# Optimization experiments

Hardware: AMD Instinct MI355X
Metric: run time of the kernel (lower is better)

## Reference

```python
import jax, jax.numpy as jnp
import numpy as np
import math

B, N, T_DIM, K, G = 4, 96, 512, 12, 8


def _normalize(x, eps=1e-6):
    n = jnp.linalg.norm(x, axis=-1, keepdims=True)
    return x / jnp.maximum(n, eps)


def setup_inputs():
    key = jax.random.key(0)
    ks = jax.random.split(key, 12)
    chest_raw = jnp.array([[-0.707, 0.0, 0.707], [0.0, 0.0, 1.0], [0.438, 0.0, 0.899],
                           [0.707, 0.0, 0.707], [0.899, 0.0, 0.438], [0.966, 0.0, 0.259]],
                          dtype=jnp.float32)
    return {
        "mu": jax.random.uniform(ks[0], (B, N), dtype=jnp.float32),
        "sigma0": jax.random.normal(ks[1], (B, N), dtype=jnp.float32) * 0.5,
        "sigma_vel": jax.random.normal(ks[2], (B, N), dtype=jnp.float32) * 0.1,
        "amplitude": jax.random.normal(ks[3], (B, N), dtype=jnp.float32),
        "sh_base": jax.random.normal(ks[4], (B, N, 9), dtype=jnp.float32) * 0.5,
        "sh_vel": jax.random.normal(ks[5], (B, N, 9), dtype=jnp.float32) * 0.1,
        "p0": jax.random.normal(ks[6], (B, N, 3), dtype=jnp.float32) * 0.5,
        "p_vel": jax.random.normal(ks[7], (B, N, 3), dtype=jnp.float32) * 0.2,
        "splat_tau_raw": jnp.asarray(0.0, dtype=jnp.float32),
        "dist_atten_raw": jnp.asarray(-0.5, dtype=jnp.float32),
        "limb_ra": jnp.zeros(3, dtype=jnp.float32),
        "limb_la": jnp.array([1.0, 0.0, 0.0], dtype=jnp.float32),
        "limb_ll": jnp.array([0.5, math.sqrt(3.0) / 2.0, 0.0], dtype=jnp.float32),
        "chest_vectors": chest_raw / jnp.linalg.norm(chest_raw, axis=-1, keepdims=True),
        "conv1_w": jax.random.normal(ks[8], (32, 2, 3, 3), dtype=jnp.float32) * 0.2,
        "conv1_b": jnp.zeros(32, dtype=jnp.float32),
        "conv2_w": jax.random.normal(ks[9], (32, 32, 3, 3), dtype=jnp.float32) * 0.06,
        "conv2_b": jnp.zeros(32, dtype=jnp.float32),
        "fc_w": jax.random.normal(ks[10], (1, 32), dtype=jnp.float32) * 0.2,
        "fc_b": jnp.zeros(1, dtype=jnp.float32),
        "T": T_DIM,
    }


def _conv3x3(x, w, b):
    y = jax.lax.conv_general_dilated(x, w, (1, 1), 'SAME',
                                     dimension_numbers=('NCHW', 'OIHW', 'NCHW'))
    return y + b[None, :, None, None]


def reference(mu, sigma0, sigma_vel, amplitude, sh_base, sh_vel, p0, p_vel,
              splat_tau_raw, dist_atten_raw, limb_ra, limb_la, limb_ll, chest_vectors,
              conv1_w, conv1_b, conv2_w, conv2_b, fc_w, fc_b, T):
    Bq, Nq = mu.shape
    # temporal Gaussian profile
    t = jnp.linspace(0.0, 1.0, T)                                   # (T,)
    dt = t[None, None, :] - mu[:, :, None]                          # (B,N,T)
    sigma_t = jax.nn.softplus(sigma0[:, :, None] + sigma_vel[:, :, None] * dt) + 1e-3
    gauss = amplitude[:, :, None] * jnp.exp(-0.5 * (dt / sigma_t) ** 2)   # (B,N,T)
    sh_dyn = sh_base[:, :, None, :] + sh_vel[:, :, None, :] * dt[..., None]  # (B,N,T,9)

    # dipole position inside the open unit ball
    p_raw = p0[:, :, None, :] + p_vel[:, :, None, :] * dt[..., None]      # (B,N,T,3)
    nrm = jnp.maximum(jnp.linalg.norm(p_raw, axis=-1, keepdims=True), 1e-8)
    p_pos = p_raw / nrm * jnp.tanh(nrm)                                   # (B,N,T,3)

    # limb lead axes from Einthoven triangle (derived every forward)
    L_I = _normalize(limb_la - limb_ra)
    L_II = _normalize(limb_ll - limb_ra)
    L_III = _normalize(limb_ll - limb_la)
    L_aVR = _normalize(limb_ra - (limb_la + limb_ll) * 0.5)
    L_aVL = _normalize(limb_la - (limb_ra + limb_ll) * 0.5)
    L_aVF = _normalize(limb_ll - (limb_ra + limb_la) * 0.5)
    limb = jnp.stack([L_I, L_II, L_III, L_aVR, L_aVL, L_aVF], 0)          # (6,3)
    chest = _normalize(chest_vectors)                                     # (6,3)
    lead = jnp.concatenate([limb, chest], 0)                              # (12,3)
    Lt = jnp.broadcast_to(lead[None, :, None, :], (Bq, 12, T, 3))         # (B,K,T,3)

    # camera-plane orthonormal basis per lead
    a1 = jnp.array([1.0, 0.0, 0.0], dtype=Lt.dtype)
    a2 = jnp.array([0.0, 1.0, 0.0], dtype=Lt.dtype)
    e1 = jnp.cross(Lt, jnp.broadcast_to(a1, Lt.shape))
    small = jnp.linalg.norm(e1, axis=-1, keepdims=True) < 1e-4
    e1 = jnp.where(small, jnp.cross(Lt, jnp.broadcast_to(a2, Lt.shape)), e1)
    e1 = _normalize(e1)
    e2 = _normalize(jnp.cross(e1, Lt))

    # project dipoles onto each lead's image plane
    u = jnp.tanh(jnp.einsum('bntc,bktc->bnkt', p_pos, e1))               # (B,N,K,T)
    v = jnp.tanh(jnp.einsum('bntc,bktc->bnkt', p_pos, e2))

    # spherical-harmonic basis evaluated at lead directions
    x_lv, y_lv, z_lv = Lt[..., 0], Lt[..., 1], Lt[..., 2]                # (B,K,T)
    Y = jnp.stack([0.282095 * jnp.ones_like(x_lv), -0.488603 * y_lv, 0.488603 * z_lv,
                   -0.488603 * x_lv, 1.092548 * x_lv * y_lv, -1.092548 * y_lv * z_lv,
                   0.315392 * (3.0 * z_lv ** 2 - 1.0), -1.092548 * x_lv * z_lv,
                   0.546274 * (x_lv ** 2 - y_lv ** 2)], axis=-1)          # (B,K,T,9)
    sh_proj = jnp.einsum('bntm,bktm->bnkt', sh_dyn, Y)                    # (B,N,K,T)

    tau = jax.nn.softplus(splat_tau_raw) + 0.06
    gamma = jax.nn.softplus(dist_atten_raw) + 1e-6
    p_nrm = jnp.maximum(jnp.linalg.norm(p_pos, axis=-1), 1e-8)            # (B,N,T)
    cosl = jnp.einsum('bntc,bktc->bnkt', p_pos, Lt) / p_nrm[:, :, None, :]
    hem = jnp.maximum(cosl, 0.0)  # halfspace gate (lead_halfspace_gate=True)
    theta = jnp.arccos(jnp.clip(cosl, -1.0 + 1e-6, 1.0 - 1e-6))
    weight = hem * jnp.exp(-gamma * theta * theta)                        # (B,N,K,T)

    # separable splat kernel: exp(-0.5((u-gx)^2+(v-gy)^2)/tau^2) = ku * kv
    grid = jnp.linspace(-1.0, 1.0, G)
    inv2tau2 = 0.5 / (tau * tau)
    ku = jnp.exp(-inv2tau2 * (u[..., None] - grid) ** 2)                  # (B,N,K,T,W)
    kv = jnp.exp(-inv2tau2 * (v[..., None] - grid) ** 2)                  # (B,N,K,T,H)

    A = gauss[:, :, None, :] * weight                                     # (B,N,K,T)
    splat_pos = jnp.einsum('bnkt,bnkth,bnktw->bkthw', A, kv, ku)          # (B,K,T,H,W)
    splat_sh = jnp.einsum('bnkt,bnkth,bnktw->bkthw', A * sh_proj, kv, ku)

    # shared CNN readout over all leads (weights shared)
    x = jnp.stack([splat_pos, splat_sh], axis=3)                          # (B,K,T,2,H,W)
    x = x.reshape(Bq * 12 * T, 2, G, G)
    h = jax.nn.gelu(_conv3x3(x, conv1_w, conv1_b), approximate=False)
    h = jax.nn.gelu(_conv3x3(h, conv2_w, conv2_b), approximate=False)
    h = h.mean(axis=(2, 3))                                               # (B*K*T, 32)
    s = h @ fc_w.T + fc_b                                                 # (B*K*T, 1)
    scalars = s.reshape(Bq, 12, T)                                        # per (b,k,t)
    # faithful to torch: cat(outs,dim=1) -> (B*T,12) then .view(B,12,T)
    V = jnp.transpose(scalars, (0, 2, 1)).reshape(Bq, 12, T)
    return V
```

## Files before the change

### kernel.cpp

```cpp
#include <hip/hip_runtime.h>

#define B_ 4
#define N_ 96
#define T_ 512
#define G_ 8
#define NIMG (B_*12*T_)

typedef _Float16 half8 __attribute__((ext_vector_type(8)));
typedef _Float16 half2t __attribute__((ext_vector_type(2)));
typedef float floatx4 __attribute__((ext_vector_type(4)));
typedef float floatx2 __attribute__((ext_vector_type(2)));

__device__ __forceinline__ float softplusf(float x) {
    return (x > 15.0f) ? x : __logf(1.0f + __expf(x));
}
__device__ __forceinline__ float softplus_small(float x) {
    return __logf(1.0f + __expf(x));
}
__device__ __forceinline__ float fast_tanhf(float x) {
    float ax = fabsf(x);
    float e  = __expf(-2.0f * ax);
    float r  = (1.0f - e) * __builtin_amdgcn_rcpf(1.0f + e);
    return copysignf(r, x);
}
__device__ __forceinline__ float tanh_pade(float x) {
    float x2 = x * x;
    float num = fmaf(x2, x2 + 105.0f, 945.0f);
    float den = fmaf(x2, fmaf(x2, 15.0f, 420.0f), 945.0f);
    return x * num * __builtin_amdgcn_rcpf(den);
}
__device__ __forceinline__ float geluf(float x) {
    float z  = 0.70710678118654752f * x;
    float az = fabsf(z);
    float t  = __builtin_amdgcn_rcpf(fmaf(0.47047f, az, 1.0f));
    float poly = t * fmaf(t, fmaf(t, 0.7478556f, -0.0958798f), 0.3480242f);
    float e  = __expf(-az * az);
    float er = fmaf(-poly, e, 1.0f);
    er = copysignf(er, z);
    return 0.5f * x * (1.0f + er);
}
__device__ __forceinline__ float rfl(float x) {
    return __int_as_float(__builtin_amdgcn_readfirstlane(__float_as_int(x)));
}

__global__ __launch_bounds__(256, 3) void splat_kernel(
    const float* __restrict__ mu,  const float* __restrict__ sg0,
    const float* __restrict__ sgv, const float* __restrict__ amp,
    const float* __restrict__ shb, const float* __restrict__ shv,
    const float* __restrict__ p0,  const float* __restrict__ pv,
    const float* __restrict__ tau_raw, const float* __restrict__ da_raw,
    const float* __restrict__ ra, const float* __restrict__ la,
    const float* __restrict__ ll, const float* __restrict__ chest,
    const float* __restrict__ w1, const float* __restrict__ w2,
    _Float16* __restrict__ outp, _Float16* __restrict__ W1p,
    _Float16* __restrict__ W2p) {
    int lx   = threadIdx.x;
    int nc   = threadIdx.y;
    int flat = nc*64 + lx;
    int tt = lx & 31, ch = lx >> 5;
    int Lb = blockIdx.x;
    int t0 = (Lb & 15) << 5;
    int k  = (Lb >> 4) % 12;
    int b  = Lb / 192;

    if (Lb < 10) {
        for (int e = Lb*1152 + flat; e < Lb*1152 + 1152; e += 256) {
            int tap = e/1280, rem = e - tap*1280, co = rem/40, ci = rem - co*40;
            float val = (ci < 32) ? w2[(co*32+ci)*9 + tap] : 0.0f;
            W2p[e] = (_Float16)val;
        }
    } else if (Lb == 10) {
        for (int e = flat; e < 32*40; e += 256) {
            int co = e/40, kk = e - co*40;
            float val = 0.0f;
            if (kk < 18) { int ci = kk & 1, tap = kk >> 1; val = w1[(co*2+ci)*9 + tap]; }
            W1p[e] = (_Float16)val;
        }
    }

    float vx, vy, vz;
    if      (k == 0) { vx = la[0]-ra[0]; vy = la[1]-ra[1]; vz = la[2]-ra[2]; }
    else if (k == 1) { vx = ll[0]-ra[0]; vy = ll[1]-ra[1]; vz = ll[2]-ra[2]; }
    else if (k == 2) { vx = ll[0]-la[0]; vy = ll[1]-la[1]; vz = ll[2]-la[2]; }
    else if (k == 3) { vx = ra[0]-0.5f*(la[0]+ll[0]); vy = ra[1]-0.5f*(la[1]+ll[1]); vz = ra[2]-0.5f*(la[2]+ll[2]); }
    else if (k == 4) { vx = la[0]-0.5f*(ra[0]+ll[0]); vy = la[1]-0.5f*(ra[1]+ll[1]); vz = la[2]-0.5f*(ra[2]+ll[2]); }
    else if (k == 5) { vx = ll[0]-0.5f*(ra[0]+la[0]); vy = ll[1]-0.5f*(ra[1]+la[1]); vz = ll[2]-0.5f*(ra[2]+la[2]); }
    else             { vx = chest[(k-6)*3+0]; vy = chest[(k-6)*3+1]; vz = chest[(k-6)*3+2]; }
    float nn = fmaxf(sqrtf(vx*vx+vy*vy+vz*vz), 1e-6f);
    float Lx = vx/nn, Ly = vy/nn, Lz = vz/nn;
    float e1x = 0.0f, e1y = Lz, e1z = -Ly;
    if (sqrtf(e1y*e1y + e1z*e1z) < 1e-4f) { e1x = -Lz; e1y = 0.0f; e1z = Lx; }
    float en = fmaxf(sqrtf(e1x*e1x+e1y*e1y+e1z*e1z), 1e-6f);
    e1x /= en; e1y /= en; e1z /= en;
    float e2x = e1y*Lz - e1z*Ly, e2y = e1z*Lx - e1x*Lz, e2z = e1x*Ly - e1y*Lx;
    float fn = fmaxf(sqrtf(e2x*e2x+e2y*e2y+e2z*e2z), 1e-6f);
    e2x /= fn; e2y /= fn; e2z /= fn;
    Lx = rfl(Lx); Ly = rfl(Ly); Lz = rfl(Lz);
    e1x = rfl(e1x); e1y = rfl(e1y); e1z = rfl(e1z);
    e2x = rfl(e2x); e2y = rfl(e2y); e2z = rfl(e2z);
    float Y[9];
    Y[0] = rfl( 0.282095f);
    Y[1] = rfl(-0.488603f*Ly);
    Y[2] = rfl( 0.488603f*Lz);
    Y[3] = rfl(-0.488603f*Lx);
    Y[4] = rfl( 1.092548f*Lx*Ly);
    Y[5] = rfl(-1.092548f*Ly*Lz);
    Y[6] = rfl( 0.315392f*fmaf(3.0f*Lz, Lz, -1.0f));
    Y[7] = rfl(-1.092548f*Lx*Lz);
    Y[8] = rfl( 0.546274f*(Lx*Lx - Ly*Ly));

    float tau = softplusf(tau_raw[0]) + 0.06f;
    float cc2 = rfl(0.5f/(tau*tau));
    float gamma = rfl(softplusf(da_raw[0]) + 1e-6f);
    const float S = 2.0f/7.0f;
    float twoccS = rfl(2.0f*cc2*S);
    float q[8];
#pragma unroll
    for (int w = 0; w < 8; ++w) { float gw = S*(float)w; q[w] = rfl(__expf(-cc2*gw*gw)); }

    float tf = (float)(t0 + tt) * (1.0f/511.0f);
    floatx2 acc2[32];
#pragma unroll
    for (int i = 0; i < 32; ++i) acc2[i] = (floatx2){0.f, 0.f};

    int n0 = nc*24;
    for (int n = n0; n < n0+24; ++n) {
        int base = b*N_ + n;
        float dt  = tf - mu[base];
        float sig = softplus_small(fmaf(sgv[base], dt, sg0[base])) + 1e-3f;
        float z   = dt * __builtin_amdgcn_rcpf(sig);
        float gauss = amp[base] * __expf(-0.5f*z*z);
        float prx = fmaf(pv[base*3+0], dt, p0[base*3+0]);
        float pry = fmaf(pv[base*3+1], dt, p0[base*3+1]);
        float prz = fmaf(pv[base*3+2], dt, p0[base*3+2]);
        float nr  = sqrtf(prx*prx + pry*pry + prz*prz);
        float ncl = fmaxf(nr, 1e-8f);
        float th  = fast_tanhf(ncl);
        float scl = th * __builtin_amdgcn_rcpf(ncl);
        float px = prx*scl, py = pry*scl, pz = prz*scl;
        float pn = fmaxf(th, 1e-8f);
        float cosl = (px*Lx + py*Ly + pz*Lz) * __builtin_amdgcn_rcpf(pn);
        float hem  = fmaxf(cosl, 0.0f);
        if (gauss != 0.0f && hem > 0.0f) {
            float c = fminf(cosl, 0.999999f);
            float s = sqrtf(1.0f - c);
            float theta = s * fmaf(c, fmaf(c, fmaf(c, -0.0187293f, 0.0742610f),
                                   -0.2121144f), 1.5707288f);
            float A = gauss * hem * __expf(-gamma*theta*theta);
            float uu = tanh_pade(px*e1x + py*e1y + pz*e1z);
            float vv = tanh_pade(px*e2x + py*e2y + pz*e2z);
            float Ach = A;
            if (ch) {
                float shp = 0.0f;
#pragma unroll
                for (int m = 0; m < 9; ++m)
                    shp += fmaf(shv[base*9+m], dt, shb[base*9+m]) * Y[m];
                Ach = A * shp;
            }
            float du = uu + 1.0f, dv = vv + 1.0f;
            float bu = __expf(-cc2*du*du);
            float bv = __expf(-cc2*dv*dv);
            float ru = __expf(twoccS*du);
            float rv = __expf(twoccS*dv);
            floatx2 ku2[4];
            float rw = bu;
#pragma unroll
            for (int w = 0; w < 8; ++w) { ku2[w>>1][w&1] = rw*q[w]; rw *= ru; }
            rw = bv;
#pragma unroll
            for (int h = 0; h < 8; ++h) {
                float tp = (rw*q[h])*Ach; rw *= rv;
                floatx2 tp2 = (floatx2){tp, tp};
#pragma unroll
                for (int w2 = 0; w2 < 4; ++w2)
                    acc2[h*4+w2] = __builtin_elementwise_fma(tp2, ku2[w2], acc2[h*4+w2]);
            }
        }
    }

    __shared__ float red[32*132];
    int rbase = tt*132 + ch*64;
    if (nc == 0) {
#pragma unroll
        for (int j = 0; j < 16; ++j) {
            floatx4 v = { acc2[2*j][0], acc2[2*j][1], acc2[2*j+1][0], acc2[2*j+1][1] };
            *(floatx4*)&red[rbase + 4*j] = v;
        }
    }
    __syncthreads();
    if (nc == 1) {
#pragma unroll
        for (int j = 0; j < 16; ++j) {
            floatx4 cur = *(const floatx4*)&red[rbase + 4*j];
            cur[0] += acc2[2*j][0]; cur[1] += acc2[2*j][1];
            cur[2] += acc2[2*j+1][0]; cur[3] += acc2[2*j+1][1];
            *(floatx4*)&red[rbase + 4*j] = cur;
        }
    }
    __syncthreads();
    if (nc == 2) {
#pragma unroll
        for (int j = 0; j < 16; ++j) {
            floatx4 cur = *(const floatx4*)&red[rbase + 4*j];
            cur[0] += acc2[2*j][0]; cur[1] += acc2[2*j][1];
            cur[2] += acc2[2*j+1][0]; cur[3] += acc2[2*j+1][1];
            *(floatx4*)&red[rbase + 4*j] = cur;
        }
    }
    __syncthreads();
    if (nc == 3) {
#pragma unroll
        for (int j = 0; j < 16; ++j) {
            floatx4 cur = *(const floatx4*)&red[rbase + 4*j];
            cur[0] += acc2[2*j][0]; cur[1] += acc2[2*j][1];
            cur[2] += acc2[2*j+1][0]; cur[3] += acc2[2*j+1][1];
            *(floatx4*)&red[rbase + 4*j] = cur;
        }
    }
    __syncthreads();

    int imgbase = (b*12 + k)*T_ + t0;
    int e0 = flat*16, r = e0 >> 7, c0 = e0 & 127;
    half8 h0, h1;
#pragma unroll
    for (int j = 0; j < 8; ++j) {
        h0[j] = (_Float16)red[r*132 + c0 + j];
        h1[j] = (_Float16)red[r*132 + c0 + 8 + j];
    }
    *(half8*)&outp[(imgbase + r)*128 + c0]     = h0;
    *(half8*)&outp[(imgbase + r)*128 + c0 + 8] = h1;
}

__global__ __launch_bounds__(192, 4) void cnn_kernel(
    const _Float16* __restrict__ splat, const _Float16* __restrict__ W1p,
    const _Float16* __restrict__ W2p,  const float* __restrict__ b1,
    const float* __restrict__ b2,      const float* __restrict__ fcw,
    const float* __restrict__ fcb,     float* __restrict__ outv) {
    __shared__ __align__(16) _Float16 sH1[3][100*40];
    __shared__ __align__(16) _Float16 sIn[3][200];
    int wv = threadIdx.y, lane = threadIdx.x;
    int img = blockIdx.x*3 + wv;
    _Float16* H  = sH1[wv];
    _Float16* IN = sIn[wv];
    {
        unsigned long long* hz = (unsigned long long*)H;
        for (int i = lane; i < 1000; i += 64) hz[i] = 0ull;
        unsigned int* iz = (unsigned int*)IN;
        for (int i = lane; i < 100; i += 64) iz[i] = 0u;
    }
#pragma unroll
    for (int ii = 0; ii < 2; ++ii) {
        int i = ii*64 + lane;
        int ci = i >> 6, p = i & 63;
        IN[(((p>>3)+1)*10 + (p&7) + 1)*2 + ci] = splat[img*128 + i];
    }

    int r = lane & 15, qd = lane >> 4;
    floatx4 b14[2], b24[2], fw4[2];
#pragma unroll
    for (int nt = 0; nt < 2; ++nt) {
        int cb = nt*16 + qd*4;
        b14[nt] = *(const floatx4*)&b1[cb];
        b24[nt] = *(const floatx4*)&b2[cb];
        fw4[nt] = *(const floatx4*)&fcw[cb];
    }

    floatx4 c1[2][4];
#pragma unroll
    for (int nt = 0; nt < 2; ++nt)
#pragma unroll
      for (int mt = 0; mt < 4; ++mt) c1[nt][mt] = b14[nt];
    half8 bw[2];
#pragma unroll
    for (int nt = 0; nt < 2; ++nt)
        bw[nt] = *(const half8*)&W1p[(nt*16+r)*40 + qd*8];
#pragma unroll
    for (int mt = 0; mt < 4; ++mt) {
        int p = mt*16 + r, py = p>>3, px = p&7;
        half8 a;
#pragma unroll
        for (int m = 0; m < 4; ++m) {
            int tap = qd*4 + m;
            int tc  = (tap > 8) ? 8 : tap;
            int ky = tc/3, kx = tc - ky*3;
            half2t pr = *(const half2t*)&IN[((py+ky)*10 + (px+kx))*2];
            if (tap >= 9) { pr[0] = (_Float16)0.0f; pr[1] = (_Float16)0.0f; }
            a[2*m]   = pr[0];
            a[2*m+1] = pr[1];
        }
#pragma unroll
        for (int nt = 0; nt < 2; ++nt)
            c1[nt][mt] = __builtin_amdgcn_mfma_f32_16x16x32_f16(bw[nt], a, c1[nt][mt], 0, 0, 0);
    }
#pragma unroll
    for (int nt = 0; nt < 2; ++nt)
#pragma unroll
      for (int mt = 0; mt < 4; ++mt) {
        int p = mt*16 + r, py = p>>3, px = p&7;
        int hb = ((py+1)*10 + (px+1))*40 + nt*16 + qd*4;
        half2t h01, h23;
        h01[0] = (_Float16)geluf(c1[nt][mt][0]);
        h01[1] = (_Float16)geluf(c1[nt][mt][1]);
        h23[0] = (_Float16)geluf(c1[nt][mt][2]);
        h23[1] = (_Float16)geluf(c1[nt][mt][3]);
        *(half2t*)&H[hb]     = h01;
        *(half2t*)&H[hb + 2] = h23;
      }

    floatx4 c2[2][4];
#pragma unroll
    for (int nt = 0; nt < 2; ++nt)
#pragma unroll
      for (int mt = 0; mt < 4; ++mt) c2[nt][mt] = b24[nt];
#pragma unroll
    for (int tap = 0; tap < 9; ++tap) {
        int ky = tap/3, kx = tap - (tap/3)*3;
        half8 wb[2];
#pragma unroll
        for (int nt = 0; nt < 2; ++nt)
            wb[nt] = *(const half8*)&W2p[tap*1280 + (nt*16+r)*40 + qd*8];
#pragma unroll
        for (int mt = 0; mt < 4; ++mt) {
            int p = mt*16 + r, py = p>>3, px = p&7;
            half8 a = *(const half8*)&H[((py+ky)*10 + (px+kx))*40 + qd*8];
#pragma unroll
            for (int nt = 0; nt < 2; ++nt)
                c2[nt][mt] = __builtin_amdgcn_mfma_f32_16x16x32_f16(wb[nt], a, c2[nt][mt], 0, 0, 0);
        }
    }
    float tot = 0.f;
#pragma unroll
    for (int nt = 0; nt < 2; ++nt)
#pragma unroll
      for (int mt = 0; mt < 4; ++mt)
#pragma unroll
        for (int j = 0; j < 4; ++j)
            tot = fmaf(geluf(c2[nt][mt][j]), fw4[nt][j], tot);
    tot *= (1.0f/64.0f);
    tot += __shfl_xor(tot, 1);  tot += __shfl_xor(tot, 2);
    tot += __shfl_xor(tot, 4);  tot += __shfl_xor(tot, 8);
    tot += __shfl_xor(tot, 16); tot += __shfl_xor(tot, 32);
    tot += fcb[0];
    if (lane == 0) {
        int t = img & 511, bk = img >> 9;
        int kk = bk % 12, bb = bk / 12;
        outv[(bb*T_ + t)*12 + kk] = tot;
    }
}

extern "C" void kernel_launch(void* const* d_in, const int* in_sizes, int n_in,
                              void* d_out, int out_size, void* d_ws, size_t ws_size,
                              hipStream_t stream) {
    const float* mu   = (const float*)d_in[0];
    const float* sg0  = (const float*)d_in[1];
    const float* sgv  = (const float*)d_in[2];
    const float* amp  = (const float*)d_in[3];
    const float* shb  = (const float*)d_in[4];
    const float* shv  = (const float*)d_in[5];
    const float* p0   = (const float*)d_in[6];
    const float* pvel = (const float*)d_in[7];
    const float* taur = (const float*)d_in[8];
    const float* dar  = (const float*)d_in[9];
    const float* ra   = (const float*)d_in[10];
    const float* la   = (const float*)d_in[11];
    const float* ll   = (const float*)d_in[12];
    const float* chest= (const float*)d_in[13];
    const float* w1   = (const float*)d_in[14];
    const float* b1   = (const float*)d_in[15];
    const float* w2   = (const float*)d_in[16];
    const float* b2   = (const float*)d_in[17];
    const float* fcw  = (const float*)d_in[18];
    const float* fcb  = (const float*)d_in[19];

    char* ws = (char*)d_ws;
    _Float16*  W1p   = (_Float16*)ws;
    _Float16*  W2p   = (_Float16*)(ws + 4096);
    _Float16*  splat = (_Float16*)(ws + 32768);

    splat_kernel<<<768, dim3(64,4), 0, stream>>>(mu, sg0, sgv, amp, shb, shv, p0, pvel,
                                                 taur, dar, ra, la, ll, chest, w1, w2,
                                                 splat, W1p, W2p);
    cnn_kernel<<<NIMG/3, dim3(64,3), 0, stream>>>(splat, W1p, W2p, b1, b2, fcw, fcb,
                                                  (float*)d_out);
}
```

Baseline: 194.4 us.

## Process four images per CNN wave with prefetched input and interleaved splat layout

Each CNN wave now handles four consecutive images instead of one, with two waves per block. This amortises the LDS zeroing, bias and weight loads, and per-block launch overhead. The next image's input is prefetched from global memory during conv2 and loaded with one packed 32-bit access per lane. The splat kernel writes its output channel-interleaved so those packed loads work, and the 1/64 mean scale is folded into the fc weights. The cost is fewer blocks in the grid and serial work per wave, which reduces the parallelism available to hide latency.

```diff
diff --git a/kernel.cpp b/kernel.cpp
--- a/kernel.cpp
+++ b/kernel.cpp
@@ -220,26 +220,29 @@
     __syncthreads();
 
     int imgbase = (b*12 + k)*T_ + t0;
-    int e0 = flat*16, r = e0 >> 7, c0 = e0 & 127;
+    int r2 = flat >> 3;
+    int pp = (flat & 7) * 8;
     half8 h0, h1;
 #pragma unroll
-    for (int j = 0; j < 8; ++j) {
-        h0[j] = (_Float16)red[r*132 + c0 + j];
-        h1[j] = (_Float16)red[r*132 + c0 + 8 + j];
-    }
-    *(half8*)&outp[(imgbase + r)*128 + c0]     = h0;
-    *(half8*)&outp[(imgbase + r)*128 + c0 + 8] = h1;
-}
-
-__global__ __launch_bounds__(192, 4) void cnn_kernel(
+    for (int j = 0; j < 4; ++j) {
+        h0[2*j]   = (_Float16)red[r2*132 + pp + j];
+        h0[2*j+1] = (_Float16)red[r2*132 + 64 + pp + j];
+        h1[2*j]   = (_Float16)red[r2*132 + pp + 4 + j];
+        h1[2*j+1] = (_Float16)red[r2*132 + 64 + pp + 4 + j];
+    }
+    *(half8*)&outp[(imgbase + r2)*128 + pp*2]     = h0;
+    *(half8*)&outp[(imgbase + r2)*128 + pp*2 + 8] = h1;
+}
+
+__global__ __launch_bounds__(128, 4) void cnn_kernel(
     const _Float16* __restrict__ splat, const _Float16* __restrict__ W1p,
     const _Float16* __restrict__ W2p,  const float* __restrict__ b1,
     const float* __restrict__ b2,      const float* __restrict__ fcw,
     const float* __restrict__ fcb,     float* __restrict__ outv) {
-    __shared__ __align__(16) _Float16 sH1[3][100*40];
-    __shared__ __align__(16) _Float16 sIn[3][200];
+    __shared__ __align__(16) _Float16 sH1[2][100*40];
+    __shared__ __align__(16) _Float16 sIn[2][200];
     int wv = threadIdx.y, lane = threadIdx.x;
-    int img = blockIdx.x*3 + wv;
+    int img0 = (blockIdx.x*2 + wv)*4;
     _Float16* H  = sH1[wv];
     _Float16* IN = sIn[wv];
     {
@@ -248,12 +251,9 @@
         unsigned int* iz = (unsigned int*)IN;
         for (int i = lane; i < 100; i += 64) iz[i] = 0u;
     }
-#pragma unroll
-    for (int ii = 0; ii < 2; ++ii) {
-        int i = ii*64 + lane;
-        int ci = i >> 6, p = i & 63;
-        IN[(((p>>3)+1)*10 + (p&7) + 1)*2 + ci] = splat[img*128 + i];
-    }
+    int pstg = lane;
+    int inoff = (((pstg>>3)+1)*10 + (pstg&7) + 1)*2;
+    *(unsigned int*)&IN[inoff] = *(const unsigned int*)&splat[img0*128 + pstg*2];
 
     int r = lane & 15, qd = lane >> 4;
     floatx4 b14[2], b24[2], fw4[2];
@@ -262,89 +262,96 @@
         int cb = nt*16 + qd*4;
         b14[nt] = *(const floatx4*)&b1[cb];
         b24[nt] = *(const floatx4*)&b2[cb];
-        fw4[nt] = *(const floatx4*)&fcw[cb];
-    }
-
-    floatx4 c1[2][4];
-#pragma unroll
-    for (int nt = 0; nt < 2; ++nt)
-#pragma unroll
-      for (int mt = 0; mt < 4; ++mt) c1[nt][mt] = b14[nt];
+        floatx4 f = *(const floatx4*)&fcw[cb];
+        f[0] *= (1.0f/64.0f); f[1] *= (1.0f/64.0f);
+        f[2] *= (1.0f/64.0f); f[3] *= (1.0f/64.0f);
+        fw4[nt] = f;
+    }
     half8 bw[2];
 #pragma unroll
     for (int nt = 0; nt < 2; ++nt)
         bw[nt] = *(const half8*)&W1p[(nt*16+r)*40 + qd*8];
-#pragma unroll
-    for (int mt = 0; mt < 4; ++mt) {
-        int p = mt*16 + r, py = p>>3, px = p&7;
-        half8 a;
-#pragma unroll
-        for (int m = 0; m < 4; ++m) {
-            int tap = qd*4 + m;
-            int tc  = (tap > 8) ? 8 : tap;
-            int ky = tc/3, kx = tc - ky*3;
-            half2t pr = *(const half2t*)&IN[((py+ky)*10 + (px+kx))*2];
-            if (tap >= 9) { pr[0] = (_Float16)0.0f; pr[1] = (_Float16)0.0f; }
-            a[2*m]   = pr[0];
-            a[2*m+1] = pr[1];
-        }
+
+    for (int it = 0; it < 4; ++it) {
+        int img = img0 + it;
+        floatx4 c1[2][4];
 #pragma unroll
         for (int nt = 0; nt < 2; ++nt)
-            c1[nt][mt] = __builtin_amdgcn_mfma_f32_16x16x32_f16(bw[nt], a, c1[nt][mt], 0, 0, 0);
-    }
-#pragma unroll
-    for (int nt = 0; nt < 2; ++nt)
-#pragma unroll
-      for (int mt = 0; mt < 4; ++mt) {
-        int p = mt*16 + r, py = p>>3, px = p&7;
-        int hb = ((py+1)*10 + (px+1))*40 + nt*16 + qd*4;
-        half2t h01, h23;
-        h01[0] = (_Float16)geluf(c1[nt][mt][0]);
-        h01[1] = (_Float16)geluf(c1[nt][mt][1]);
-        h23[0] = (_Float16)geluf(c1[nt][mt][2]);
-        h23[1] = (_Float16)geluf(c1[nt][mt][3]);
-        *(half2t*)&H[hb]     = h01;
-        *(half2t*)&H[hb + 2] = h23;
-      }
-
-    floatx4 c2[2][4];
-#pragma unroll
-    for (int nt = 0; nt < 2; ++nt)
-#pragma unroll
-      for (int mt = 0; mt < 4; ++mt) c2[nt][mt] = b24[nt];
-#pragma unroll
-    for (int tap = 0; tap < 9; ++tap) {
-        int ky = tap/3, kx = tap - (tap/3)*3;
-        half8 wb[2];
-#pragma unroll
-        for (int nt = 0; nt < 2; ++nt)
-            wb[nt] = *(const half8*)&W2p[tap*1280 + (nt*16+r)*40 + qd*8];
+#pragma unroll
+          for (int mt = 0; mt < 4; ++mt) c1[nt][mt] = b14[nt];
 #pragma unroll
         for (int mt = 0; mt < 4; ++mt) {
             int p = mt*16 + r, py = p>>3, px = p&7;
-            half8 a = *(const half8*)&H[((py+ky)*10 + (px+kx))*40 + qd*8];
+            half8 a;
+#pragma unroll
+            for (int m = 0; m < 4; ++m) {
+                int tap = qd*4 + m;
+                int tc  = (tap > 8) ? 8 : tap;
+                int ky = tc/3, kx = tc - ky*3;
+                half2t pr = *(const half2t*)&IN[((py+ky)*10 + (px+kx))*2];
+                if (tap >= 9) { pr[0] = (_Float16)0.0f; pr[1] = (_Float16)0.0f; }
+                a[2*m]   = pr[0];
+                a[2*m+1] = pr[1];
+            }
 #pragma unroll
             for (int nt = 0; nt < 2; ++nt)
-                c2[nt][mt] = __builtin_amdgcn_mfma_f32_16x16x32_f16(wb[nt], a, c2[nt][mt], 0, 0, 0);
-        }
-    }
-    float tot = 0.f;
-#pragma unroll
-    for (int nt = 0; nt < 2; ++nt)
-#pragma unroll
-      for (int mt = 0; mt < 4; ++mt)
-#pragma unroll
-        for (int j = 0; j < 4; ++j)
-            tot = fmaf(geluf(c2[nt][mt][j]), fw4[nt][j], tot);
-    tot *= (1.0f/64.0f);
-    tot += __shfl_xor(tot, 1);  tot += __shfl_xor(tot, 2);
-    tot += __shfl_xor(tot, 4);  tot += __shfl_xor(tot, 8);
-    tot += __shfl_xor(tot, 16); tot += __shfl_xor(tot, 32);
-    tot += fcb[0];
-    if (lane == 0) {
-        int t = img & 511, bk = img >> 9;
-        int kk = bk % 12, bb = bk / 12;
-        outv[(bb*T_ + t)*12 + kk] = tot;
+                c1[nt][mt] = __builtin_amdgcn_mfma_f32_16x16x32_f16(bw[nt], a, c1[nt][mt], 0, 0, 0);
+        }
+        unsigned int nxt = 0u;
+        if (it < 3) nxt = *(const unsigned int*)&splat[(img+1)*128 + pstg*2];
+#pragma unroll
+        for (int nt = 0; nt < 2; ++nt)
+#pragma unroll
+          for (int mt = 0; mt < 4; ++mt) {
+            int p = mt*16 + r, py = p>>3, px = p&7;
+            int hb = ((py+1)*10 + (px+1))*40 + nt*16 + qd*4;
+            half2t h01, h23;
+            h01[0] = (_Float16)geluf(c1[nt][mt][0]);
+            h01[1] = (_Float16)geluf(c1[nt][mt][1]);
+            h23[0] = (_Float16)geluf(c1[nt][mt][2]);
+            h23[1] = (_Float16)geluf(c1[nt][mt][3]);
+            *(half2t*)&H[hb]     = h01;
+            *(half2t*)&H[hb + 2] = h23;
+          }
+        floatx4 c2[2][4];
+#pragma unroll
+        for (int nt = 0; nt < 2; ++nt)
+#pragma unroll
+          for (int mt = 0; mt < 4; ++mt) c2[nt][mt] = b24[nt];
+#pragma unroll
+        for (int tap = 0; tap < 9; ++tap) {
+            int ky = tap/3, kx = tap - (tap/3)*3;
+            half8 wb[2];
+#pragma unroll
+            for (int nt = 0; nt < 2; ++nt)
+                wb[nt] = *(const half8*)&W2p[tap*1280 + (nt*16+r)*40 + qd*8];
+#pragma unroll
+            for (int mt = 0; mt < 4; ++mt) {
+                int p = mt*16 + r, py = p>>3, px = p&7;
+                half8 a = *(const half8*)&H[((py+ky)*10 + (px+kx))*40 + qd*8];
+#pragma unroll
+                for (int nt = 0; nt < 2; ++nt)
+                    c2[nt][mt] = __builtin_amdgcn_mfma_f32_16x16x32_f16(wb[nt], a, c2[nt][mt], 0, 0, 0);
+            }
+        }
+        if (it < 3) *(unsigned int*)&IN[inoff] = nxt;
+        float tot = 0.f;
+#pragma unroll
+        for (int nt = 0; nt < 2; ++nt)
+#pragma unroll
+          for (int mt = 0; mt < 4; ++mt)
+#pragma unroll
+            for (int j = 0; j < 4; ++j)
+                tot = fmaf(geluf(c2[nt][mt][j]), fw4[nt][j], tot);
+        tot += __shfl_xor(tot, 1);  tot += __shfl_xor(tot, 2);
+        tot += __shfl_xor(tot, 4);  tot += __shfl_xor(tot, 8);
+        tot += __shfl_xor(tot, 16); tot += __shfl_xor(tot, 32);
+        tot += fcb[0];
+        if (lane == 0) {
+            int t = img & 511, bk = img >> 9;
+            int kk = bk % 12, bb = bk / 12;
+            outv[(bb*T_ + t)*12 + kk] = tot;
+        }
     }
 }
 
@@ -380,6 +387,6 @@
     splat_kernel<<<768, dim3(64,4), 0, stream>>>(mu, sg0, sgv, amp, shb, shv, p0, pvel,
                                                  taur, dar, ra, la, ll, chest, w1, w2,
                                                  splat, W1p, W2p);
-    cnn_kernel<<<NIMG/3, dim3(64,3), 0, stream>>>(splat, W1p, W2p, b1, b2, fcw, fcb,
+    cnn_kernel<<<NIMG/8, dim3(64,2), 0, stream>>>(splat, W1p, W2p, b1, b2, fcw, fcb,
                                                   (float*)d_out);
 }
```

New measurement: 282.0 us. +45.1%, slower.
